# Kernel optimization log

Measured on AMD Instinct MI355X. Metric: run time of the kernel, lower is better.

## Reference

```python
import jax, jax.numpy as jnp
import numpy as np

N = 50000
E = 600000
D = 128
EPS = 1e-5  # nn.LayerNorm default eps


def gcn_conv(x, W, b, src, dst):
    # PyG GCNConv with add_self_loops=True, edge_weight=None (all ones),
    # symmetric normalization D^-1/2 (A+I) D^-1/2.
    h = x @ W                                        # [N, D]
    deg = jnp.zeros((N,), h.dtype).at[dst].add(1.0) + 1.0  # +1 for self loop
    dinv = jax.lax.rsqrt(deg)                        # deg >= 1, safe
    norm = dinv[src] * dinv[dst]                     # [E]
    msg = h[src] * norm[:, None]                     # [E, D] gather
    agg = jax.ops.segment_sum(msg, dst, num_segments=N)
    agg = agg + h * (dinv * dinv)[:, None]           # self-loop term
    return agg + b


def layer_norm(x, g, b):
    mu = jnp.mean(x, axis=-1, keepdims=True)
    var = jnp.mean(jnp.square(x - mu), axis=-1, keepdims=True)
    return (x - mu) * jax.lax.rsqrt(var + EPS) * g + b


def setup_inputs() -> dict:
    key = jax.random.key(0)
    ks = jax.random.split(key, 6)
    x = jax.random.normal(ks[0], (N, D), dtype=jnp.float32)
    edge_index = jax.random.randint(ks[1], (2, E), 0, N, dtype=jnp.int64)
    s = 1.0 / np.sqrt(D)
    W1 = jax.random.uniform(ks[2], (D, D), jnp.float32, -s, s)
    W2 = jax.random.uniform(ks[3], (D, D), jnp.float32, -s, s)
    b1 = jnp.zeros((D,), jnp.float32)
    b2 = jnp.zeros((D,), jnp.float32)
    ln1_g = jnp.ones((D,), jnp.float32)
    ln1_b = jnp.zeros((D,), jnp.float32)
    ln2_g = jnp.ones((D,), jnp.float32)
    ln2_b = jnp.zeros((D,), jnp.float32)
    return {"x": x, "edge_index": edge_index, "W1": W1, "b1": b1,
            "ln1_g": ln1_g, "ln1_b": ln1_b, "W2": W2, "b2": b2,
            "ln2_g": ln2_g, "ln2_b": ln2_b}


def reference(x, edge_index, W1, b1, ln1_g, ln1_b, W2, b2, ln2_g, ln2_b):
    src, dst = edge_index[0], edge_index[1]
    out = gcn_conv(x, W1, b1, src, dst)
    out = jax.nn.relu(layer_norm(out, ln1_g, ln1_b))  # dropout = identity (eval)
    out = gcn_conv(out, W2, b2, src, dst)
    out = jax.nn.relu(layer_norm(out, ln2_g, ln2_b))
    return out + x
```

## Files before the change

### kernel.cpp

```cpp
#include <hip/hip_runtime.h>
#include <hip/hip_fp16.h>

#define D 128
#define EPS 1e-5f
#define KB 64
#define NBSH 7
#define BUCKW 128

typedef unsigned int u32;
typedef unsigned short u16;
typedef unsigned char u8;
typedef __attribute__((ext_vector_type(8))) _Float16 half8;
typedef __attribute__((ext_vector_type(4))) float f32x4;
typedef __attribute__((ext_vector_type(2))) float f32x2;

__device__ inline u16 f2h(float x) {
  _Float16 t = (_Float16)x;
  return __builtin_bit_cast(u16, t);
}
__device__ inline u8 f2fp8(float x) {
  return (u8)(__builtin_amdgcn_cvt_pk_fp8_f32(x, x, 0, false) & 0xff);
}

__global__ __launch_bounds__(256) void k_prep(const float* __restrict__ W1,
                                              const float* __restrict__ W2,
                                              u16* __restrict__ Wt1,
                                              u16* __restrict__ Wt2) {
  int i = blockIdx.x * 256 + threadIdx.x;
  if (i < 2 * D * D) {
    const float* W = (i < D * D) ? W1 : W2;
    u16* Wt = (i < D * D) ? Wt1 : Wt2;
    int ii = i & (D * D - 1);
    int k = ii >> 7, c = ii & 127;
    Wt[c * D + k] = f2h(W[ii]);
  }
}

template <bool F32IN>
__device__ __forceinline__ void gemm_body(const void* __restrict__ in_,
                                          const u16* __restrict__ Wt,
                                          u8* __restrict__ out, int nrows,
                                          int blk) {
  const int tid = threadIdx.x;
  const int lane = tid & 63, wv = tid >> 6;
  const int m = lane & 15, q = lane >> 4;
  const int r0 = blk * 64 + wv * 16;
  const int rowa = min(r0 + m, nrows - 1);

  f32x4 acc[8];
#pragma unroll
  for (int ct = 0; ct < 8; ct++) acc[ct] = (f32x4)(0.0f);

#pragma unroll
  for (int kk = 0; kk < 4; kk++) {
    const int kbase = kk * 32 + q * 8;
    half8 a;
    if (F32IN) {
      const float* in = (const float*)in_;
      float4 v0 = *(const float4*)(in + (size_t)rowa * D + kbase);
      float4 v1 = *(const float4*)(in + (size_t)rowa * D + kbase + 4);
      a[0] = (_Float16)v0.x; a[1] = (_Float16)v0.y;
      a[2] = (_Float16)v0.z; a[3] = (_Float16)v0.w;
      a[4] = (_Float16)v1.x; a[5] = (_Float16)v1.y;
      a[6] = (_Float16)v1.z; a[7] = (_Float16)v1.w;
    } else {
      const u16* in = (const u16*)in_;
      a = *(const half8*)(in + (size_t)rowa * D + kbase);
    }
#pragma unroll
    for (int ct = 0; ct < 8; ct++) {
      half8 b = *(const half8*)(Wt + (ct * 16 + m) * D + kbase);
      acc[ct] = __builtin_amdgcn_mfma_f32_16x16x32_f16(a, b, acc[ct], 0, 0, 0);
    }
  }

#pragma unroll
  for (int ct = 0; ct < 8; ct++) {
#pragma unroll
    for (int rg = 0; rg < 4; rg++) {
      int rr = r0 + q * 4 + rg;
      if (rr < nrows) out[(size_t)rr * D + ct * 16 + m] = f2fp8(acc[ct][rg]);
    }
  }
}

__global__ __launch_bounds__(256) void k_count_gemm1(
    const int* __restrict__ dst, int* __restrict__ cnt, int E, int NB, int EPB,
    const float* __restrict__ x, const u16* __restrict__ Wt1,
    u8* __restrict__ A, int nrows) {
  if (blockIdx.x < (u32)KB) {
    __shared__ int hist[512];
    const int k = blockIdx.x, tid = threadIdx.x;
    for (int i = tid; i < NB; i += 256) hist[i] = 0;
    __syncthreads();
    const int e0 = k * EPB, e1 = min(E, e0 + EPB);
    for (int base = e0 + tid; base < e1; base += 2048) {
      int dd[8];
#pragma unroll
      for (int i = 0; i < 8; i++) {
        int e = base + i * 256;
        dd[i] = (e < e1) ? dst[e] : -1;
      }
#pragma unroll
      for (int i = 0; i < 8; i++)
        if (dd[i] >= 0) atomicAdd(&hist[dd[i] >> NBSH], 1);
    }
    __syncthreads();
    for (int b = tid; b < NB; b += 256) cnt[b * KB + k] = hist[b];
  } else {
    gemm_body<true>(x, Wt1, A, nrows, blockIdx.x - KB);
  }
}

__global__ __launch_bounds__(1024) void k_scan(int* __restrict__ cnt, int M,
                                               int NB, int* __restrict__ bsv,
                                               int E) {
  __shared__ int wt[16];
  const int tid = threadIdx.x;
  const int lane = tid & 63, wid = tid >> 6;
  const int chunks = (M + 1023) >> 10;
  int running = 0;
  int i = tid;
  int v = (i < M) ? cnt[i] : 0;
  for (int c = 0; c < chunks; c++) {
    int inext = i + 1024;
    int vnext = (c + 1 < chunks && inext < M) ? cnt[inext] : 0;
    int incl = v;
#pragma unroll
    for (int o = 1; o < 64; o <<= 1) {
      int t = __shfl_up(incl, o, 64);
      if (lane >= o) incl += t;
    }
    if (lane == 63) wt[wid] = incl;
    __syncthreads();
    int woff = 0, total = 0;
#pragma unroll
    for (int j = 0; j < 16; j++) {
      int t = wt[j];
      if (j < wid) woff += t;
      total += t;
    }
    int excl = running + woff + incl - v;
    if (i < M) {
      cnt[i] = excl;
      if ((i & (KB - 1)) == 0) bsv[i / KB] = excl;
    }
    running += total;
    __syncthreads();
    i = inext;
    v = vnext;
  }
  if (tid == 0) bsv[NB] = E;
}

__global__ __launch_bounds__(256) void k_scatter(
    const int* __restrict__ src, const int* __restrict__ dst,
    const int* __restrict__ cnt, u32* __restrict__ tmp, int E, int NB,
    int EPB) {
  __shared__ int off[512];
  const int k = blockIdx.x, tid = threadIdx.x;
  for (int b = tid; b < NB; b += 256) off[b] = cnt[b * KB + k];
  __syncthreads();
  const int e0 = k * EPB, e1 = min(E, e0 + EPB);
  for (int base = e0 + tid; base < e1; base += 2048) {
    int dd[8], ss[8];
#pragma unroll
    for (int i = 0; i < 8; i++) {
      int e = base + i * 256;
      dd[i] = (e < e1) ? dst[e] : -1;
      ss[i] = (e < e1) ? src[e] : 0;
    }
#pragma unroll
    for (int i = 0; i < 8; i++) {
      if (dd[i] >= 0) {
        int p = atomicAdd(&off[dd[i] >> NBSH], 1);
        tmp[p] = (u32)ss[i] | ((u32)(dd[i] & (BUCKW - 1)) << 16);
      }
    }
  }
}

__global__ __launch_bounds__(256) void k_bucket(
    const u32* __restrict__ tmp, const int* __restrict__ bsv,
    int4* __restrict__ meta, float* __restrict__ dinv,
    u32* __restrict__ csr, int N) {
  __shared__ int hist[BUCKW];
  __shared__ int sc[BUCKW];
  __shared__ int cur[BUCKW];
  const int b = blockIdx.x, tid = threadIdx.x;
  const int s0 = bsv[b], s1 = bsv[b + 1];
  if (tid < BUCKW) hist[tid] = 0;
  __syncthreads();
  for (int base = s0 + tid; base < s1; base += 1024) {
    int tt[4];
#pragma unroll
    for (int i = 0; i < 4; i++) {
      int idx = base + i * 256;
      tt[i] = (idx < s1) ? (int)tmp[idx] : -1;
    }
#pragma unroll
    for (int i = 0; i < 4; i++)
      if (tt[i] >= 0) atomicAdd(&hist[(tt[i] >> 16) & (BUCKW - 1)], 1);
  }
  __syncthreads();
  if (tid < BUCKW) sc[tid] = hist[tid];
  __syncthreads();
#pragma unroll
  for (int o = 1; o < BUCKW; o <<= 1) {
    int t = 0;
    if (tid < BUCKW && tid >= o) t = sc[tid - o];
    __syncthreads();
    if (tid < BUCKW) sc[tid] += t;
    __syncthreads();
  }
  if (tid < BUCKW) {
    int dg = hist[tid];
    int excl = sc[tid] - dg;
    cur[tid] = excl;
    int d = (b << NBSH) + tid;
    if (d < N) {
      float dv = rsqrtf((float)dg + 1.0f);
      meta[d] = make_int4(s0 + excl, dg, __builtin_bit_cast(int, dv), 0);
      dinv[d] = dv;
    }
  }
  __syncthreads();
  for (int base = s0 + tid; base < s1; base += 1024) {
    int tt[4];
#pragma unroll
    for (int i = 0; i < 4; i++) {
      int idx = base + i * 256;
      tt[i] = (idx < s1) ? (int)tmp[idx] : -1;
    }
#pragma unroll
    for (int i = 0; i < 4; i++) {
      if (tt[i] >= 0) {
        int r = atomicAdd(&cur[(tt[i] >> 16) & (BUCKW - 1)], 1);
        csr[s0 + r] = (u32)tt[i] & 0xffffu;
      }
    }
  }
}

__global__ __launch_bounds__(256) void k_weights(
    const int4* __restrict__ meta, const float* __restrict__ dinv,
    u32* __restrict__ csr, int N) {
  int gid = blockIdx.x * 256 + threadIdx.x;
  int r = gid >> 2, j0 = gid & 3;
  if (r >= N) return;
  int4 mt = meta[r];
  float dv = __builtin_bit_cast(float, mt.z);
  for (int j = j0; j < mt.y; j += 4) {
    u32 s = csr[mt.x + j];
    float w = dinv[s] * dv;
    csr[mt.x + j] = s | ((u32)f2h(w) << 16);
  }
}

__device__ __forceinline__ void gather_ln_core(
    const uint2* __restrict__ hb, const int4* __restrict__ meta,
    const u32* __restrict__ csr, const float* __restrict__ b,
    const float* __restrict__ g, const float* __restrict__ bln,
    int row, int n, int sl, float out[8]) {
  const bool valid = row < n;
  const int rc = valid ? row : 0;
  int4 mt = meta[rc];
  int beg = mt.x;
  int cnt = valid ? mt.y : 0;
  float dv = __builtin_bit_cast(float, mt.z);
  float sn = dv * dv;

  float acc[8];
  {
    uint2 su = hb[(size_t)rc * 16 + sl];
    f32x2 p0 = __builtin_amdgcn_cvt_pk_f32_fp8(su.x, false);
    f32x2 p1 = __builtin_amdgcn_cvt_pk_f32_fp8(su.x, true);
    f32x2 p2 = __builtin_amdgcn_cvt_pk_f32_fp8(su.y, false);
    f32x2 p3 = __builtin_amdgcn_cvt_pk_f32_fp8(su.y, true);
    acc[0] = p0[0] * sn; acc[1] = p0[1] * sn;
    acc[2] = p1[0] * sn; acc[3] = p1[1] * sn;
    acc[4] = p2[0] * sn; acc[5] = p2[1] * sn;
    acc[6] = p3[0] * sn; acc[7] = p3[1] * sn;
  }

  int cm = max(cnt, __shfl_xor(cnt, 16, 64));
  cm = max(cm, __shfl_xor(cm, 32, 64));

  for (int j0 = 0; j0 < cm; j0 += 16) {
    u32 e = 0u;
    if (sl < cnt - j0) e = csr[beg + j0 + sl];
    int mm = min(cm - j0, 16);
    for (int j = 0; j < mm; j += 4) {
      u32 e0 = __shfl(e, j, 16),     e1 = __shfl(e, j + 1, 16);
      u32 e2 = __shfl(e, j + 2, 16), e3 = __shfl(e, j + 3, 16);
      uint2 v0 = hb[(size_t)(e0 & 0xffffu) * 16 + sl];
      uint2 v1 = hb[(size_t)(e1 & 0xffffu) * 16 + sl];
      uint2 v2 = hb[(size_t)(e2 & 0xffffu) * 16 + sl];
      uint2 v3 = hb[(size_t)(e3 & 0xffffu) * 16 + sl];
      float w0 = (float)__builtin_bit_cast(_Float16, (u16)(e0 >> 16));
      float w1 = (float)__builtin_bit_cast(_Float16, (u16)(e1 >> 16));
      float w2 = (float)__builtin_bit_cast(_Float16, (u16)(e2 >> 16));
      float w3 = (float)__builtin_bit_cast(_Float16, (u16)(e3 >> 16));
      f32x2 p;
      p = __builtin_amdgcn_cvt_pk_f32_fp8(v0.x, false);
      acc[0] = fmaf(p[0], w0, acc[0]); acc[1] = fmaf(p[1], w0, acc[1]);
      p = __builtin_amdgcn_cvt_pk_f32_fp8(v0.x, true);
      acc[2] = fmaf(p[0], w0, acc[2]); acc[3] = fmaf(p[1], w0, acc[3]);
      p = __builtin_amdgcn_cvt_pk_f32_fp8(v0.y, false);
      acc[4] = fmaf(p[0], w0, acc[4]); acc[5] = fmaf(p[1], w0, acc[5]);
      p = __builtin_amdgcn_cvt_pk_f32_fp8(v0.y, true);
      acc[6] = fmaf(p[0], w0, acc[6]); acc[7] = fmaf(p[1], w0, acc[7]);

      p = __builtin_amdgcn_cvt_pk_f32_fp8(v1.x, false);
      acc[0] = fmaf(p[0], w1, acc[0]); acc[1] = fmaf(p[1], w1, acc[1]);
      p = __builtin_amdgcn_cvt_pk_f32_fp8(v1.x, true);
      acc[2] = fmaf(p[0], w1, acc[2]); acc[3] = fmaf(p[1], w1, acc[3]);
      p = __builtin_amdgcn_cvt_pk_f32_fp8(v1.y, false);
      acc[4] = fmaf(p[0], w1, acc[4]); acc[5] = fmaf(p[1], w1, acc[5]);
      p = __builtin_amdgcn_cvt_pk_f32_fp8(v1.y, true);
      acc[6] = fmaf(p[0], w1, acc[6]); acc[7] = fmaf(p[1], w1, acc[7]);

      p = __builtin_amdgcn_cvt_pk_f32_fp8(v2.x, false);
      acc[0] = fmaf(p[0], w2, acc[0]); acc[1] = fmaf(p[1], w2, acc[1]);
      p = __builtin_amdgcn_cvt_pk_f32_fp8(v2.x, true);
      acc[2] = fmaf(p[0], w2, acc[2]); acc[3] = fmaf(p[1], w2, acc[3]);
      p = __builtin_amdgcn_cvt_pk_f32_fp8(v2.y, false);
      acc[4] = fmaf(p[0], w2, acc[4]); acc[5] = fmaf(p[1], w2, acc[5]);
      p = __builtin_amdgcn_cvt_pk_f32_fp8(v2.y, true);
      acc[6] = fmaf(p[0], w2, acc[6]); acc[7] = fmaf(p[1], w2, acc[7]);

      p = __builtin_amdgcn_cvt_pk_f32_fp8(v3.x, false);
      acc[0] = fmaf(p[0], w3, acc[0]); acc[1] = fmaf(p[1], w3, acc[1]);
      p = __builtin_amdgcn_cvt_pk_f32_fp8(v3.x, true);
      acc[2] = fmaf(p[0], w3, acc[2]); acc[3] = fmaf(p[1], w3, acc[3]);
      p = __builtin_amdgcn_cvt_pk_f32_fp8(v3.y, false);
      acc[4] = fmaf(p[0], w3, acc[4]); acc[5] = fmaf(p[1], w3, acc[5]);
      p = __builtin_amdgcn_cvt_pk_f32_fp8(v3.y, true);
      acc[6] = fmaf(p[0], w3, acc[6]); acc[7] = fmaf(p[1], w3, acc[7]);
    }
  }

  int d0 = sl * 8;
  float4 bb0 = *(const float4*)(b + d0);
  float4 bb1 = *(const float4*)(b + d0 + 4);
  float a0 = acc[0] + bb0.x, a1 = acc[1] + bb0.y;
  float a2 = acc[2] + bb0.z, a3 = acc[3] + bb0.w;
  float a4 = acc[4] + bb1.x, a5 = acc[5] + bb1.y;
  float a6 = acc[6] + bb1.z, a7 = acc[7] + bb1.w;

  float sum = ((a0 + a1) + (a2 + a3)) + ((a4 + a5) + (a6 + a7));
#pragma unroll
  for (int o = 8; o >= 1; o >>= 1) sum += __shfl_xor(sum, o, 16);
  float mu = sum * (1.0f / 128.0f);
  float e0 = a0 - mu, e1 = a1 - mu, e2 = a2 - mu, e3 = a3 - mu;
  float e4 = a4 - mu, e5 = a5 - mu, e6 = a6 - mu, e7 = a7 - mu;
  float vs = ((e0 * e0 + e1 * e1) + (e2 * e2 + e3 * e3)) +
             ((e4 * e4 + e5 * e5) + (e6 * e6 + e7 * e7));
#pragma unroll
  for (int o = 8; o >= 1; o >>= 1) vs += __shfl_xor(vs, o, 16);
  float inv = rsqrtf(vs * (1.0f / 128.0f) + EPS);

  float4 gg0 = *(const float4*)(g + d0);
  float4 gg1 = *(const float4*)(g + d0 + 4);
  float4 bl0 = *(const float4*)(bln + d0);
  float4 bl1 = *(const float4*)(bln + d0 + 4);
  out[0] = fmaxf(e0 * inv * gg0.x + bl0.x, 0.0f);
  out[1] = fmaxf(e1 * inv * gg0.y + bl0.y, 0.0f);
  out[2] = fmaxf(e2 * inv * gg0.z + bl0.z, 0.0f);
  out[3] = fmaxf(e3 * inv * gg0.w + bl0.w, 0.0f);
  out[4] = fmaxf(e4 * inv * gg1.x + bl1.x, 0.0f);
  out[5] = fmaxf(e5 * inv * gg1.y + bl1.y, 0.0f);
  out[6] = fmaxf(e6 * inv * gg1.z + bl1.z, 0.0f);
  out[7] = fmaxf(e7 * inv * gg1.w + bl1.w, 0.0f);
}

__global__ __launch_bounds__(256) void k_mid(
    const uint2* __restrict__ hb, const int4* __restrict__ meta,
    const u32* __restrict__ csr,
    const float* __restrict__ b, const float* __restrict__ g,
    const float* __restrict__ bln,
    const u16* __restrict__ Wt2, u8* __restrict__ outB, int n) {
  __shared__ alignas(16) u16 sY[64 * 136];
  const int tid = threadIdx.x;
  const int sl = tid & 15;
  const int row0 = blockIdx.x * 64;

  for (int p = 0; p < 4; p++) {
    int lr = p * 16 + (tid >> 4);
    int row = row0 + lr;
    float o[8];
    gather_ln_core(hb, meta, csr, b, g, bln, row, n, sl, o);
    uint4 pk;
    pk.x = ((u32)f2h(o[1]) << 16) | (u32)f2h(o[0]);
    pk.y = ((u32)f2h(o[3]) << 16) | (u32)f2h(o[2]);
    pk.z = ((u32)f2h(o[5]) << 16) | (u32)f2h(o[4]);
    pk.w = ((u32)f2h(o[7]) << 16) | (u32)f2h(o[6]);
    *(uint4*)(sY + lr * 136 + sl * 8) = pk;
  }
  __syncthreads();

  const int lane = tid & 63, wv = tid >> 6;
  const int m = lane & 15, q = lane >> 4;
  f32x4 acc[8];
#pragma unroll
  for (int ct = 0; ct < 8; ct++) acc[ct] = (f32x4)(0.0f);
  const u16* ap = sY + (wv * 16 + m) * 136 + q * 8;
#pragma unroll
  for (int kk = 0; kk < 4; kk++) {
    half8 a = *(const half8*)(ap + kk * 32);
#pragma unroll
    for (int ct = 0; ct < 8; ct++) {
      half8 bfr = *(const half8*)(Wt2 + (ct * 16 + m) * D + kk * 32 + q * 8);
      acc[ct] = __builtin_amdgcn_mfma_f32_16x16x32_f16(a, bfr, acc[ct], 0, 0, 0);
    }
  }
#pragma unroll
  for (int ct = 0; ct < 8; ct++) {
#pragma unroll
    for (int rg = 0; rg < 4; rg++) {
      int rr = row0 + wv * 16 + q * 4 + rg;
      if (rr < n) outB[(size_t)rr * D + ct * 16 + m] = f2fp8(acc[ct][rg]);
    }
  }
}

__global__ __launch_bounds__(256) void k_gather2(
    const uint2* __restrict__ hb, const int4* __restrict__ meta,
    const u32* __restrict__ csr,
    const float* __restrict__ b, const float* __restrict__ g,
    const float* __restrict__ bln, const float* __restrict__ resid,
    float* __restrict__ outf, int n) {
  const int tid = threadIdx.x;
  const int sl = tid & 15;
  const int row = blockIdx.x * 16 + (tid >> 4);
  float o[8];
  gather_ln_core(hb, meta, csr, b, g, bln, row, n, sl, o);
  if (row >= n) return;
  size_t base = (size_t)row * D + sl * 8;
  float4 r0 = *(const float4*)(resid + base);
  float4 r1 = *(const float4*)(resid + base + 4);
  *(float4*)(outf + base) =
      make_float4(o[0] + r0.x, o[1] + r0.y, o[2] + r0.z, o[3] + r0.w);
  *(float4*)(outf + base + 4) =
      make_float4(o[4] + r1.x, o[5] + r1.y, o[6] + r1.z, o[7] + r1.w);
}

extern "C" void kernel_launch(void* const* d_in, const int* in_sizes, int n_in,
                              void* d_out, int out_size, void* d_ws, size_t ws_size,
                              hipStream_t stream) {
  const float* x    = (const float*)d_in[0];
  const int*   ei   = (const int*)d_in[1];
  const float* W1   = (const float*)d_in[2];
  const float* b1   = (const float*)d_in[3];
  const float* g1   = (const float*)d_in[4];
  const float* bl1  = (const float*)d_in[5];
  const float* W2   = (const float*)d_in[6];
  const float* b2   = (const float*)d_in[7];
  const float* g2   = (const float*)d_in[8];
  const float* bl2  = (const float*)d_in[9];

  const int N = in_sizes[0] / D;
  const int E = in_sizes[1] / 2;
  const int* src = ei;
  const int* dst = ei + E;

  const int NB  = (N + BUCKW - 1) / BUCKW;
  const int M   = NB * KB;
  const int EPB = (E + KB - 1) / KB;
  const int GB  = (N + 63) / 64;

  size_t off = 0;
  auto walloc = [&](size_t bytes) {
    void* p = (char*)d_ws + off;
    off = (off + bytes + 255) & ~(size_t)255;
    return p;
  };
  int*   cnt   = (int*)walloc((size_t)M * 4);
  int*   bsv   = (int*)walloc((size_t)(NB + 1) * 4);
  u32*   tmp   = (u32*)walloc((size_t)E * 4);
  u32*   csr   = (u32*)walloc((size_t)E * 4);
  int4*  meta  = (int4*)walloc((size_t)N * 16);
  float* dinv  = (float*)walloc((size_t)N * 4);
  u8*    A     = (u8*)walloc((size_t)N * D);
  u8*    B     = (u8*)walloc((size_t)N * D);
  u16*   Wt1   = (u16*)walloc((size_t)D * D * 2);
  u16*   Wt2   = (u16*)walloc((size_t)D * D * 2);
  float* O     = (float*)d_out;

  k_prep<<<(2 * D * D + 255) / 256, 256, 0, stream>>>(W1, W2, Wt1, Wt2);
  k_count_gemm1<<<KB + GB, 256, 0, stream>>>(dst, cnt, E, NB, EPB, x, Wt1, A, N);
  k_scan<<<1, 1024, 0, stream>>>(cnt, M, NB, bsv, E);
  k_scatter<<<KB, 256, 0, stream>>>(src, dst, cnt, tmp, E, NB, EPB);
  k_bucket<<<NB, 256, 0, stream>>>(tmp, bsv, meta, dinv, csr, N);
  k_weights<<<(N * 4 + 255) / 256, 256, 0, stream>>>(meta, dinv, csr, N);
  k_mid<<<GB, 256, 0, stream>>>((const uint2*)A, meta, csr, b1, g1, bl1,
                                Wt2, B, N);
  k_gather2<<<(N + 15) / 16, 256, 0, stream>>>((const uint2*)B, meta, csr,
                                               b2, g2, bl2, x, O, N);
}
```

Measured before the change: 217.8 us.

## Prefetch CSR indices, gather eight neighbors per step, widen k_mid to 512 threads

The neighbor gather now prefetches the next 16-entry CSR chunk while the current one is processed. Each inner step issues eight independent row loads instead of four, giving more memory-level parallelism for the random feature gathers. k_mid moves to 512-thread blocks, so each block gathers 64 rows in two passes instead of four, and each wave computes half the output columns of the GEMM. The cost is higher register pressure from the wider unroll and prefetch, which may lower occupancy.

```diff
diff --git a/kernel.cpp b/kernel.cpp
--- a/kernel.cpp
+++ b/kernel.cpp
@@ -257,6 +257,19 @@
   }
 }
 
+#define ACC_EDGE(vv, ww)                                                     \
+  {                                                                          \
+    f32x2 p_;                                                                \
+    p_ = __builtin_amdgcn_cvt_pk_f32_fp8(vv.x, false);                       \
+    acc[0] = fmaf(p_[0], ww, acc[0]); acc[1] = fmaf(p_[1], ww, acc[1]);      \
+    p_ = __builtin_amdgcn_cvt_pk_f32_fp8(vv.x, true);                        \
+    acc[2] = fmaf(p_[0], ww, acc[2]); acc[3] = fmaf(p_[1], ww, acc[3]);      \
+    p_ = __builtin_amdgcn_cvt_pk_f32_fp8(vv.y, false);                       \
+    acc[4] = fmaf(p_[0], ww, acc[4]); acc[5] = fmaf(p_[1], ww, acc[5]);      \
+    p_ = __builtin_amdgcn_cvt_pk_f32_fp8(vv.y, true);                        \
+    acc[6] = fmaf(p_[0], ww, acc[6]); acc[7] = fmaf(p_[1], ww, acc[7]);      \
+  }
+
 __device__ __forceinline__ void gather_ln_core(
     const uint2* __restrict__ hb, const int4* __restrict__ meta,
     const u32* __restrict__ csr, const float* __restrict__ b,
@@ -286,57 +299,46 @@
   int cm = max(cnt, __shfl_xor(cnt, 16, 64));
   cm = max(cm, __shfl_xor(cm, 32, 64));
 
+  u32 epre = 0u;
+  if (sl < cnt) epre = csr[beg + sl];
+
   for (int j0 = 0; j0 < cm; j0 += 16) {
-    u32 e = 0u;
-    if (sl < cnt - j0) e = csr[beg + j0 + sl];
+    u32 ecur = epre;
+    epre = 0u;
+    {
+      int nj = j0 + 16;
+      if (nj < cm && sl < cnt - nj) epre = csr[beg + nj + sl];
+    }
     int mm = min(cm - j0, 16);
-    for (int j = 0; j < mm; j += 4) {
-      u32 e0 = __shfl(e, j, 16),     e1 = __shfl(e, j + 1, 16);
-      u32 e2 = __shfl(e, j + 2, 16), e3 = __shfl(e, j + 3, 16);
+    for (int j = 0; j < mm; j += 8) {
+      u32 e0 = __shfl(ecur, j + 0, 16), e1 = __shfl(ecur, j + 1, 16);
+      u32 e2 = __shfl(ecur, j + 2, 16), e3 = __shfl(ecur, j + 3, 16);
+      u32 e4 = __shfl(ecur, j + 4, 16), e5 = __shfl(ecur, j + 5, 16);
+      u32 e6 = __shfl(ecur, j + 6, 16), e7 = __shfl(ecur, j + 7, 16);
       uint2 v0 = hb[(size_t)(e0 & 0xffffu) * 16 + sl];
       uint2 v1 = hb[(size_t)(e1 & 0xffffu) * 16 + sl];
       uint2 v2 = hb[(size_t)(e2 & 0xffffu) * 16 + sl];
       uint2 v3 = hb[(size_t)(e3 & 0xffffu) * 16 + sl];
+      uint2 v4 = hb[(size_t)(e4 & 0xffffu) * 16 + sl];
+      uint2 v5 = hb[(size_t)(e5 & 0xffffu) * 16 + sl];
+      uint2 v6 = hb[(size_t)(e6 & 0xffffu) * 16 + sl];
+      uint2 v7 = hb[(size_t)(e7 & 0xffffu) * 16 + sl];
       float w0 = (float)__builtin_bit_cast(_Float16, (u16)(e0 >> 16));
       float w1 = (float)__builtin_bit_cast(_Float16, (u16)(e1 >> 16));
       float w2 = (float)__builtin_bit_cast(_Float16, (u16)(e2 >> 16));
       float w3 = (float)__builtin_bit_cast(_Float16, (u16)(e3 >> 16));
-      f32x2 p;
-      p = __builtin_amdgcn_cvt_pk_f32_fp8(v0.x, false);
-      acc[0] = fmaf(p[0], w0, acc[0]); acc[1] = fmaf(p[1], w0, acc[1]);
-      p = __builtin_amdgcn_cvt_pk_f32_fp8(v0.x, true);
-      acc[2] = fmaf(p[0], w0, acc[2]); acc[3] = fmaf(p[1], w0, acc[3]);
-      p = __builtin_amdgcn_cvt_pk_f32_fp8(v0.y, false);
-      acc[4] = fmaf(p[0], w0, acc[4]); acc[5] = fmaf(p[1], w0, acc[5]);
-      p = __builtin_amdgcn_cvt_pk_f32_fp8(v0.y, true);
-      acc[6] = fmaf(p[0], w0, acc[6]); acc[7] = fmaf(p[1], w0, acc[7]);
-
-      p = __builtin_amdgcn_cvt_pk_f32_fp8(v1.x, false);
-      acc[0] = fmaf(p[0], w1, acc[0]); acc[1] = fmaf(p[1], w1, acc[1]);
-      p = __builtin_amdgcn_cvt_pk_f32_fp8(v1.x, true);
-      acc[2] = fmaf(p[0], w1, acc[2]); acc[3] = fmaf(p[1], w1, acc[3]);
-      p = __builtin_amdgcn_cvt_pk_f32_fp8(v1.y, false);
-      acc[4] = fmaf(p[0], w1, acc[4]); acc[5] = fmaf(p[1], w1, acc[5]);
-      p = __builtin_amdgcn_cvt_pk_f32_fp8(v1.y, true);
-      acc[6] = fmaf(p[0], w1, acc[6]); acc[7] = fmaf(p[1], w1, acc[7]);
-
-      p = __builtin_amdgcn_cvt_pk_f32_fp8(v2.x, false);
-      acc[0] = fmaf(p[0], w2, acc[0]); acc[1] = fmaf(p[1], w2, acc[1]);
-      p = __builtin_amdgcn_cvt_pk_f32_fp8(v2.x, true);
-      acc[2] = fmaf(p[0], w2, acc[2]); acc[3] = fmaf(p[1], w2, acc[3]);
-      p = __builtin_amdgcn_cvt_pk_f32_fp8(v2.y, false);
-      acc[4] = fmaf(p[0], w2, acc[4]); acc[5] = fmaf(p[1], w2, acc[5]);
-      p = __builtin_amdgcn_cvt_pk_f32_fp8(v2.y, true);
-      acc[6] = fmaf(p[0], w2, acc[6]); acc[7] = fmaf(p[1], w2, acc[7]);
-
-      p = __builtin_amdgcn_cvt_pk_f32_fp8(v3.x, false);
-      acc[0] = fmaf(p[0], w3, acc[0]); acc[1] = fmaf(p[1], w3, acc[1]);
-      p = __builtin_amdgcn_cvt_pk_f32_fp8(v3.x, true);
-      acc[2] = fmaf(p[0], w3, acc[2]); acc[3] = fmaf(p[1], w3, acc[3]);
-      p = __builtin_amdgcn_cvt_pk_f32_fp8(v3.y, false);
-      acc[4] = fmaf(p[0], w3, acc[4]); acc[5] = fmaf(p[1], w3, acc[5]);
-      p = __builtin_amdgcn_cvt_pk_f32_fp8(v3.y, true);
-      acc[6] = fmaf(p[0], w3, acc[6]); acc[7] = fmaf(p[1], w3, acc[7]);
+      float w4 = (float)__builtin_bit_cast(_Float16, (u16)(e4 >> 16));
+      float w5 = (float)__builtin_bit_cast(_Float16, (u16)(e5 >> 16));
+      float w6 = (float)__builtin_bit_cast(_Float16, (u16)(e6 >> 16));
+      float w7 = (float)__builtin_bit_cast(_Float16, (u16)(e7 >> 16));
+      ACC_EDGE(v0, w0);
+      ACC_EDGE(v1, w1);
+      ACC_EDGE(v2, w2);
+      ACC_EDGE(v3, w3);
+      ACC_EDGE(v4, w4);
+      ACC_EDGE(v5, w5);
+      ACC_EDGE(v6, w6);
+      ACC_EDGE(v7, w7);
     }
   }
 
@@ -374,7 +376,7 @@
   out[7] = fmaxf(e7 * inv * gg1.w + bl1.w, 0.0f);
 }
 
-__global__ __launch_bounds__(256) void k_mid(
+__global__ __launch_bounds__(512) void k_mid(
     const uint2* __restrict__ hb, const int4* __restrict__ meta,
     const u32* __restrict__ csr,
     const float* __restrict__ b, const float* __restrict__ g,
@@ -385,8 +387,8 @@
   const int sl = tid & 15;
   const int row0 = blockIdx.x * 64;
 
-  for (int p = 0; p < 4; p++) {
-    int lr = p * 16 + (tid >> 4);
+  for (int p = 0; p < 2; p++) {
+    int lr = p * 32 + (tid >> 4);
     int row = row0 + lr;
     float o[8];
     gather_ln_core(hb, meta, csr, b, g, bln, row, n, sl, o);
@@ -401,25 +403,29 @@
 
   const int lane = tid & 63, wv = tid >> 6;
   const int m = lane & 15, q = lane >> 4;
-  f32x4 acc[8];
-#pragma unroll
-  for (int ct = 0; ct < 8; ct++) acc[ct] = (f32x4)(0.0f);
-  const u16* ap = sY + (wv * 16 + m) * 136 + q * 8;
+  const int rt = wv & 3;
+  const int ch = wv >> 2;
+  f32x4 acc[4];
+#pragma unroll
+  for (int c = 0; c < 4; c++) acc[c] = (f32x4)(0.0f);
+  const u16* ap = sY + (rt * 16 + m) * 136 + q * 8;
 #pragma unroll
   for (int kk = 0; kk < 4; kk++) {
     half8 a = *(const half8*)(ap + kk * 32);
 #pragma unroll
-    for (int ct = 0; ct < 8; ct++) {
+    for (int c = 0; c < 4; c++) {
+      int ct = ch * 4 + c;
       half8 bfr = *(const half8*)(Wt2 + (ct * 16 + m) * D + kk * 32 + q * 8);
-      acc[ct] = __builtin_amdgcn_mfma_f32_16x16x32_f16(a, bfr, acc[ct], 0, 0, 0);
-    }
-  }
-#pragma unroll
-  for (int ct = 0; ct < 8; ct++) {
+      acc[c] = __builtin_amdgcn_mfma_f32_16x16x32_f16(a, bfr, acc[c], 0, 0, 0);
+    }
+  }
+#pragma unroll
+  for (int c = 0; c < 4; c++) {
+    int ct = ch * 4 + c;
 #pragma unroll
     for (int rg = 0; rg < 4; rg++) {
-      int rr = row0 + wv * 16 + q * 4 + rg;
-      if (rr < n) outB[(size_t)rr * D + ct * 16 + m] = f2fp8(acc[ct][rg]);
+      int rr = row0 + rt * 16 + q * 4 + rg;
+      if (rr < n) outB[(size_t)rr * D + ct * 16 + m] = f2fp8(acc[c][rg]);
     }
   }
 }
@@ -493,7 +499,7 @@
   k_scatter<<<KB, 256, 0, stream>>>(src, dst, cnt, tmp, E, NB, EPB);
   k_bucket<<<NB, 256, 0, stream>>>(tmp, bsv, meta, dinv, csr, N);
   k_weights<<<(N * 4 + 255) / 256, 256, 0, stream>>>(meta, dinv, csr, N);
-  k_mid<<<GB, 256, 0, stream>>>((const uint2*)A, meta, csr, b1, g1, bl1,
+  k_mid<<<GB, 512, 0, stream>>>((const uint2*)A, meta, csr, b1, g1, bl1,
                                 Wt2, B, N);
   k_gather2<<<(N + 15) / 16, 256, 0, stream>>>((const uint2*)B, meta, csr,
                                                b2, g2, bl2, x, O, N);
```

Result: no change. 214.4 us (-1.6%).
